# Kernel optimization log

Hardware: AMD Instinct MI355X
Metric: run time of the kernel (lower is better)

## Reference

```python
import jax, jax.numpy as jnp
import numpy as np

DIAG_MASK = 1e20  # value added on the diagonal to exclude self as negative


def setup_inputs() -> dict:
    key = jax.random.key(0)
    k1, k2, k3 = jax.random.split(key, 3)
    B, D_in, D_out = 4096, 1024, 1024
    anchor_x = jax.random.normal(k1, (B, D_in), dtype=jnp.float32)
    pos_x = jax.random.normal(k2, (B, D_in), dtype=jnp.float32)
    W = jax.random.normal(k3, (D_in, D_out), dtype=jnp.float32) * (1.0 / np.sqrt(D_in))
    b = jnp.zeros((D_out,), dtype=jnp.float32)
    return {"anchor_x": anchor_x, "pos_x": pos_x, "W": W, "b": b}


def reference(anchor_x, pos_x, W, b):
    # Encoder: simple dense projection (stand-in for the wrapped BERT encoder).
    anchor = anchor_x @ W + b          # [B, D]
    pos = pos_x @ W + b                # [B, D]

    # Pairwise squared distances dist[i,j] = ||anchor_i - pos_j||^2,
    # computed via the GEMM identity |a|^2 + |p|^2 - 2 a.p (same math as the
    # original broadcasted (a_i - p_j)^2 reduce_sum, far less memory traffic).
    a2 = jnp.sum(anchor * anchor, axis=-1, keepdims=True)       # [B, 1]
    p2 = jnp.sum(pos * pos, axis=-1, keepdims=True).T           # [1, B]
    dist = a2 + p2 - 2.0 * (anchor @ pos.T)                     # [B, B]

    B = dist.shape[0]
    mask_dist = dist + jnp.eye(B, dtype=dist.dtype) * DIAG_MASK  # mask diagonal
    indices = jnp.argmin(mask_dist, axis=-1)                     # [B] hard negatives
    neg = pos[indices]                                           # gather [B, D]

    return jnp.concatenate([anchor, pos, neg], axis=-1)          # [B, 3D]
```

## Files before the change

kernel.cpp:

```cpp
#include <hip/hip_runtime.h>


typedef short s8v __attribute__((ext_vector_type(8)));
typedef _Float16 h8v __attribute__((ext_vector_type(8)));
typedef float f4v __attribute__((ext_vector_type(4)));
typedef unsigned short u16;

#define B  4096
#define D  1024
#define OLD 3072
#define OLD16 6144
#define LDK 68

__device__ __forceinline__ u16 f2bf(float f) {
  union { float f; unsigned u; } v; v.f = f;
  unsigned r = v.u + 0x7FFFu + ((v.u >> 16) & 1u);
  return (u16)(r >> 16);
}
__device__ __forceinline__ float bf2f(u16 s) {
  union { unsigned u; float f; } v; v.u = ((unsigned)s) << 16;
  return v.f;
}

__device__ __forceinline__ void gld16(const void* g, void* l) {
  __builtin_amdgcn_global_load_lds(
      (const __attribute__((address_space(1))) unsigned int*)g,
      (__attribute__((address_space(3))) unsigned int*)l, 16, 0, 0);
}

struct Top2 { float v1, v2; int j1, j2; };
__device__ __forceinline__ void t2_insert(Top2& t, float v, int j) {
  if (v < t.v1 || (v == t.v1 && j < t.j1)) {
    t.v2 = t.v1; t.j2 = t.j1; t.v1 = v; t.j1 = j;
  } else if (v < t.v2 || (v == t.v2 && j < t.j2)) {
    t.v2 = v; t.j2 = j;
  }
}
struct Top4 { float v[4]; int j[4]; };
__device__ __forceinline__ void t4_insert(Top4& t, float v, int j) {
  if (v < t.v[3] || (v == t.v[3] && j < t.j[3])) {
    int p = 3;
#pragma unroll
    for (int s = 0; s < 3; ++s) {
      if (p > 0 && (v < t.v[p - 1] || (v == t.v[p - 1] && j < t.j[p - 1]))) {
        t.v[p] = t.v[p - 1]; t.j[p] = t.j[p - 1]; --p;
      }
    }
    t.v[p] = v; t.j[p] = j;
  }
}

__global__ void splitT_W(const float* __restrict__ W, u16* __restrict__ WtQ) {
  __shared__ float tile[32][33];
  const int bx = blockIdx.x * 32, by = blockIdx.y * 32;
  const int tx = threadIdx.x, ty = threadIdx.y;
  for (int dy = 0; dy < 32; dy += 8)
    tile[ty + dy][tx] = W[(size_t)(by + ty + dy) * D + bx + tx];
  __syncthreads();
  for (int dy = 0; dy < 32; dy += 8) {
    const float v = tile[tx][ty + dy];
    const u16 h = f2bf(v);
    const size_t o = (size_t)(bx + ty + dy) * 2048 + by + tx;
    WtQ[o] = h;
    WtQ[o + 1024] = f2bf(v - bf2f(h));
  }
}

__global__ __launch_bounds__(256) void splitX2(
    const float* __restrict__ A, const float* __restrict__ P,
    u16* __restrict__ O16, u16* __restrict__ posXq) {
  const int r = blockIdx.x, t = threadIdx.x;
  const bool isPos = r >= B;
  const int row = isPos ? r - B : r;
  const float4 v = *(const float4*)&(isPos ? P : A)[(size_t)row * D + t * 4];
  const float vv[4] = {v.x, v.y, v.z, v.w};
  ushort4 hi, mi;
  u16* hp = &hi.x; u16* mp = &mi.x;
#pragma unroll
  for (int i = 0; i < 4; ++i) {
    hp[i] = f2bf(vv[i]);
    mp[i] = f2bf(vv[i] - bf2f(hp[i]));
  }
  if (isPos) {
    *(ushort4*)&posXq[(size_t)row * 2048 + t * 4] = hi;
    *(ushort4*)&posXq[(size_t)row * 2048 + 1024 + t * 4] = mi;
  } else {
    *(ushort4*)&O16[(size_t)row * OLD16 + 4096 + t * 4] = hi;
    *(ushort4*)&O16[(size_t)row * OLD16 + 5120 + t * 4] = mi;
  }
}

__global__ __launch_bounds__(256) void enc_mfma(
    float* out, const u16* __restrict__ posXq, const u16* __restrict__ WtQ,
    const float* __restrict__ bias, _Float16* __restrict__ Aq,
    _Float16* __restrict__ Pq) {
  __shared__ __align__(16) u16 lAh[2][128 * 32], lAm[2][128 * 32];
  __shared__ __align__(16) u16 lBh[2][128 * 32], lBm[2][128 * 32];
  const u16* O16 = (const u16*)out;
  const int tid = threadIdx.x, lane = tid & 63, wave = tid >> 6;
  const int waveM = wave >> 1, waveN = wave & 1;
  const int row16 = lane & 15, quad = lane >> 4;
  const bool isPos = blockIdx.y >= 32;
  const int Mbase = (blockIdx.y & 31) * 128;
  const int Nbase = blockIdx.x * 128;
  f4v acc[4][4] = {};

  auto STAGE = [&](int buf, int kk) {
#pragma unroll
    for (int i = 0; i < 2; ++i) {
      const int c = i * 256 + tid;
      const int row = c >> 2;
      const int col8 = ((c & 3) ^ ((row >> 1) & 3)) * 8;
      u16* ah = &lAh[buf][(i * 256 + wave * 64) * 8];
      u16* am = &lAm[buf][(i * 256 + wave * 64) * 8];
      u16* bh = &lBh[buf][(i * 256 + wave * 64) * 8];
      u16* bm = &lBm[buf][(i * 256 + wave * 64) * 8];
      if (isPos) {
        gld16(&posXq[(size_t)(Mbase + row) * 2048 + kk + col8], ah);
        gld16(&posXq[(size_t)(Mbase + row) * 2048 + 1024 + kk + col8], am);
      } else {
        gld16(&O16[(size_t)(Mbase + row) * OLD16 + 4096 + kk + col8], ah);
        gld16(&O16[(size_t)(Mbase + row) * OLD16 + 5120 + kk + col8], am);
      }
      gld16(&WtQ[(size_t)(Nbase + row) * 2048 + kk + col8], bh);
      gld16(&WtQ[(size_t)(Nbase + row) * 2048 + 1024 + kk + col8], bm);
    }
  };

  STAGE(0, 0);
  __syncthreads();
  int cur = 0;
  const int slot = (quad ^ ((row16 >> 1) & 3)) * 8;
  for (int t = 1; t <= 32; ++t) {
    if (t < 32) STAGE(cur ^ 1, t * 32);
    s8v ah[4], am[4], bh[4], bm[4];
#pragma unroll
    for (int mi = 0; mi < 4; ++mi) {
      const int ro = (waveM * 64 + mi * 16 + row16) * 32 + slot;
      ah[mi] = *(const s8v*)&lAh[cur][ro];
      am[mi] = *(const s8v*)&lAm[cur][ro];
    }
#pragma unroll
    for (int ni = 0; ni < 4; ++ni) {
      const int ro = (waveN * 64 + ni * 16 + row16) * 32 + slot;
      bh[ni] = *(const s8v*)&lBh[cur][ro];
      bm[ni] = *(const s8v*)&lBm[cur][ro];
    }
#pragma unroll
    for (int mi = 0; mi < 4; ++mi)
#pragma unroll
      for (int ni = 0; ni < 4; ++ni) {
        f4v a = acc[mi][ni];
        a = __builtin_amdgcn_mfma_f32_16x16x32_bf16(ah[mi], bh[ni], a, 0, 0, 0);
        a = __builtin_amdgcn_mfma_f32_16x16x32_bf16(ah[mi], bm[ni], a, 0, 0, 0);
        a = __builtin_amdgcn_mfma_f32_16x16x32_bf16(am[mi], bh[ni], a, 0, 0, 0);
        acc[mi][ni] = a;
      }
    __syncthreads();
    cur ^= 1;
  }
  const int outOff = isPos ? 1024 : 0;
  _Float16* Q = isPos ? Pq : Aq;
#pragma unroll
  for (int ni = 0; ni < 4; ++ni) {
    const int col = Nbase + waveN * 64 + ni * 16 + row16;
    const float bv = bias[col];
#pragma unroll
    for (int mi = 0; mi < 4; ++mi) {
      const int rbase = Mbase + waveM * 64 + mi * 16 + quad * 4;
#pragma unroll
      for (int r = 0; r < 4; ++r) {
        const size_t row = rbase + r;
        const float v = acc[mi][ni][r] + bv;
        out[row * OLD + outOff + col] = v;
        Q[row * 1024 + col] = (_Float16)v;
      }
    }
  }
}

__global__ __launch_bounds__(256) void pnorm(float* __restrict__ o) {
  const int row = blockIdx.x, t = threadIdx.x;
  const float4 v = *(const float4*)&o[(size_t)row * OLD + D + t * 4];
  float s = v.x * v.x + v.y * v.y + v.z * v.z + v.w * v.w;
#pragma unroll
  for (int off = 32; off; off >>= 1) s += __shfl_down(s, off, 64);
  __shared__ float wsum[4];
  if ((t & 63) == 0) wsum[t >> 6] = s;
  __syncthreads();
  if (t == 0) o[(size_t)row * OLD + 2048] = wsum[0] + wsum[1] + wsum[2] + wsum[3];
}

__global__ __launch_bounds__(256) void dist_mfma(
    const _Float16* __restrict__ Aq, const _Float16* __restrict__ Pq,
    float* __restrict__ o) {
  __shared__ __align__(16) u16 lA[2][128 * 32];
  __shared__ __align__(16) u16 lB[2][128 * 32];
  __shared__ float sv1[128][2], sv2[128][2];
  __shared__ int sj1[128][2], sj2[128][2];
  const int tid = threadIdx.x, lane = tid & 63, wave = tid >> 6;
  const int waveM = wave >> 1, waveN = wave & 1;
  const int row16 = lane & 15, quad = lane >> 4;
  const int Mbase = blockIdx.y * 128;
  const int Nbase = blockIdx.x * 128;
  f4v acc[4][4] = {};

  auto STAGE = [&](int buf, int kk) {
#pragma unroll
    for (int i = 0; i < 2; ++i) {
      const int c = i * 256 + tid;
      const int row = c >> 2;
      const int col8 = ((c & 3) ^ ((row >> 1) & 3)) * 8;
      u16* la = &lA[buf][(i * 256 + wave * 64) * 8];
      u16* lb = &lB[buf][(i * 256 + wave * 64) * 8];
      gld16(&Aq[(size_t)(Mbase + row) * 1024 + kk + col8], la);
      gld16(&Pq[(size_t)(Nbase + row) * 1024 + kk + col8], lb);
    }
  };

  STAGE(0, 0);
  __syncthreads();
  int cur = 0;
  const int slot = (quad ^ ((row16 >> 1) & 3)) * 8;
  for (int t = 1; t <= 32; ++t) {
    if (t < 32) STAGE(cur ^ 1, t * 32);
    h8v a[4], b[4];
#pragma unroll
    for (int i = 0; i < 4; ++i) {
      a[i] = *(const h8v*)&lA[cur][(waveM * 64 + i * 16 + row16) * 32 + slot];
      b[i] = *(const h8v*)&lB[cur][(waveN * 64 + i * 16 + row16) * 32 + slot];
    }
#pragma unroll
    for (int mi = 0; mi < 4; ++mi)
#pragma unroll
      for (int ni = 0; ni < 4; ++ni)
        acc[mi][ni] =
            __builtin_amdgcn_mfma_f32_16x16x32_f16(a[mi], b[ni], acc[mi][ni], 0, 0, 0);
    __syncthreads();
    cur ^= 1;
  }

  float p2c[4];
#pragma unroll
  for (int ni = 0; ni < 4; ++ni)
    p2c[ni] = o[(size_t)(Nbase + waveN * 64 + ni * 16 + row16) * OLD + 2048];
#pragma unroll
  for (int mi = 0; mi < 4; ++mi)
#pragma unroll
    for (int r = 0; r < 4; ++r) {
      const int rg = Mbase + waveM * 64 + mi * 16 + quad * 4 + r;
      Top2 tp; tp.v1 = 3.0e38f; tp.v2 = 3.0e38f; tp.j1 = 0; tp.j2 = 1;
#pragma unroll
      for (int ni = 0; ni < 4; ++ni) {
        const int cg = Nbase + waveN * 64 + ni * 16 + row16;
        if (cg != rg) t2_insert(tp, p2c[ni] - 2.0f * acc[mi][ni][r], cg);
      }
#pragma unroll
      for (int m = 1; m < 16; m <<= 1) {
        const float ov1 = __shfl_xor(tp.v1, m, 64);
        const int oj1 = __shfl_xor(tp.j1, m, 64);
        const float ov2 = __shfl_xor(tp.v2, m, 64);
        const int oj2 = __shfl_xor(tp.j2, m, 64);
        t2_insert(tp, ov1, oj1);
        t2_insert(tp, ov2, oj2);
      }
      if (row16 == 0) {
        const int rl = waveM * 64 + mi * 16 + quad * 4 + r;
        sv1[rl][waveN] = tp.v1; sj1[rl][waveN] = tp.j1;
        sv2[rl][waveN] = tp.v2; sj2[rl][waveN] = tp.j2;
      }
    }
  __syncthreads();
  if (tid < 128) {
    Top2 tp; tp.v1 = sv1[tid][0]; tp.j1 = sj1[tid][0];
    tp.v2 = sv2[tid][0]; tp.j2 = sj2[tid][0];
    t2_insert(tp, sv1[tid][1], sj1[tid][1]);
    t2_insert(tp, sv2[tid][1], sj2[tid][1]);
    ((float4*)&o[(size_t)(Mbase + tid) * OLD + 2056])[blockIdx.x] =
        make_float4(tp.v1, __int_as_float(tp.j1), tp.v2, __int_as_float(tp.j2));
  }
}

__global__ __launch_bounds__(256) void argmin_refine(float* __restrict__ o) {
  const int i = blockIdx.x, t = threadIdx.x;
  __shared__ int gj[4];
  if (t < 64) {
    Top4 tp;
#pragma unroll
    for (int c = 0; c < 4; ++c) { tp.v[c] = 3.0e38f; tp.j[c] = 0; }
    if (t < 32) {
      const float4 p = ((const float4*)&o[(size_t)i * OLD + 2056])[t];
      t4_insert(tp, p.x, __float_as_int(p.y));
      t4_insert(tp, p.z, __float_as_int(p.w));
    }
#pragma unroll
    for (int m = 1; m < 32; m <<= 1) {
#pragma unroll
      for (int c = 0; c < 4; ++c) {
        const float ov = __shfl_xor(tp.v[c], m, 64);
        const int oj = __shfl_xor(tp.j[c], m, 64);
        t4_insert(tp, ov, oj);
      }
    }
    if (t == 0) {
#pragma unroll
      for (int c = 0; c < 4; ++c)
        gj[c] = (tp.j[c] < 0) ? 0 : (tp.j[c] > B - 1 ? B - 1 : tp.j[c]);
    }
  }
  __syncthreads();
  int jj[4];
#pragma unroll
  for (int c = 0; c < 4; ++c) jj[c] = gj[c];
  const float4 a4 = *(const float4*)&o[(size_t)i * OLD + t * 4];
  float s[4], n[4];
#pragma unroll
  for (int c = 0; c < 4; ++c) {
    const float4 q = *(const float4*)&o[(size_t)jj[c] * OLD + D + t * 4];
    s[c] = a4.x * q.x + a4.y * q.y + a4.z * q.z + a4.w * q.w;
    n[c] = q.x * q.x + q.y * q.y + q.z * q.z + q.w * q.w;
  }
#pragma unroll
  for (int off = 32; off; off >>= 1)
#pragma unroll
    for (int c = 0; c < 4; ++c) {
      s[c] += __shfl_down(s[c], off, 64);
      n[c] += __shfl_down(n[c], off, 64);
    }
  __shared__ float wsum[4][8];
  __shared__ int sjf;
  if ((t & 63) == 0)
#pragma unroll
    for (int c = 0; c < 4; ++c) {
      wsum[t >> 6][c] = s[c];
      wsum[t >> 6][4 + c] = n[c];
    }
  __syncthreads();
  if (t == 0) {
    float bd = 3.4e38f; int bj = 0x7fffffff;
#pragma unroll
    for (int c = 0; c < 4; ++c) {
      const float S = wsum[0][c] + wsum[1][c] + wsum[2][c] + wsum[3][c];
      const float N = wsum[0][4 + c] + wsum[1][4 + c] + wsum[2][4 + c] + wsum[3][4 + c];
      const float d = N - 2.0f * S;
      const int j = jj[c];
      if (d < bd || (d == bd && j < bj)) { bd = d; bj = j; }
    }
    sjf = bj;
  }
  __syncthreads();
  const int j = sjf;
  ((float4*)&o[(size_t)i * OLD + 2048])[t] = ((const float4*)&o[(size_t)j * OLD + D])[t];
}

__global__ __launch_bounds__(256) void enc_gemm(
    const float* __restrict__ X, const float* __restrict__ W,
    const float* __restrict__ bia, float* __restrict__ out, int outOff) {
  __shared__ float lA[32][LDK];
  __shared__ float lW[32][LDK];
  const int tid = threadIdx.x;
  const int Mbase = blockIdx.y * 64;
  const int Nbase = blockIdx.x * 64;
  const int ty = tid >> 4, tx = tid & 15;
  float acc[4][4] = {};
  for (int k0 = 0; k0 < D; k0 += 32) {
    __syncthreads();
#pragma unroll
    for (int h = 0; h < 2; ++h) {
      const int ch = tid + h * 256;
      const int r = ch >> 3, c4 = (ch & 7) * 4;
      const float4 a4 = *(const float4*)&X[(size_t)(Mbase + r) * D + k0 + c4];
      lA[c4 + 0][r] = a4.x; lA[c4 + 1][r] = a4.y;
      lA[c4 + 2][r] = a4.z; lA[c4 + 3][r] = a4.w;
      const int kr = ch >> 4, nc = (ch & 15) * 4;
      *(float4*)&lW[kr][nc] = *(const float4*)&W[(size_t)(k0 + kr) * D + Nbase + nc];
    }
    __syncthreads();
#pragma unroll
    for (int kk = 0; kk < 32; ++kk) {
      const float4 av = *(const float4*)&lA[kk][ty * 4];
      const float4 wv = *(const float4*)&lW[kk][tx * 4];
      acc[0][0] += av.x * wv.x; acc[0][1] += av.x * wv.y; acc[0][2] += av.x * wv.z; acc[0][3] += av.x * wv.w;
      acc[1][0] += av.y * wv.x; acc[1][1] += av.y * wv.y; acc[1][2] += av.y * wv.z; acc[1][3] += av.y * wv.w;
      acc[2][0] += av.z * wv.x; acc[2][1] += av.z * wv.y; acc[2][2] += av.z * wv.z; acc[2][3] += av.z * wv.w;
      acc[3][0] += av.w * wv.x; acc[3][1] += av.w * wv.y; acc[3][2] += av.w * wv.z; acc[3][3] += av.w * wv.w;
    }
  }
  const float4 b4 = *(const float4*)&bia[Nbase + tx * 4];
#pragma unroll
  for (int i = 0; i < 4; ++i) {
    const int row = Mbase + ty * 4 + i;
    float4 ov;
    ov.x = acc[i][0] + b4.x; ov.y = acc[i][1] + b4.y;
    ov.z = acc[i][2] + b4.z; ov.w = acc[i][3] + b4.w;
    *(float4*)&out[(size_t)row * OLD + outOff + Nbase + tx * 4] = ov;
  }
}

__global__ __launch_bounds__(256) void dist_argmin_f32(float* __restrict__ o) {
  __shared__ float lA[32][LDK];
  __shared__ float lB[32][LDK];
  const int tid = threadIdx.x;
  const int Mbase = blockIdx.y * 64, Nbase = blockIdx.x * 64;
  const int ty = tid >> 4, tx = tid & 15;
  float acc[4][4] = {};
  for (int k0 = 0; k0 < D; k0 += 32) {
    __syncthreads();
#pragma unroll
    for (int h = 0; h < 2; ++h) {
      const int ch = tid + h * 256;
      const int r = ch >> 3, c4 = (ch & 7) * 4;
      const float4 a4 = *(const float4*)&o[(size_t)(Mbase + r) * OLD + k0 + c4];
      const float4 b4 = *(const float4*)&o[(size_t)(Nbase + r) * OLD + D + k0 + c4];
      lA[c4 + 0][r] = a4.x; lA[c4 + 1][r] = a4.y;
      lA[c4 + 2][r] = a4.z; lA[c4 + 3][r] = a4.w;
      lB[c4 + 0][r] = b4.x; lB[c4 + 1][r] = b4.y;
      lB[c4 + 2][r] = b4.z; lB[c4 + 3][r] = b4.w;
    }
    __syncthreads();
#pragma unroll
    for (int kk = 0; kk < 32; ++kk) {
      const float4 av = *(const float4*)&lA[kk][ty * 4];
      const float4 bv = *(const float4*)&lB[kk][tx * 4];
      acc[0][0] += av.x * bv.x; acc[0][1] += av.x * bv.y; acc[0][2] += av.x * bv.z; acc[0][3] += av.x * bv.w;
      acc[1][0] += av.y * bv.x; acc[1][1] += av.y * bv.y; acc[1][2] += av.y * bv.z; acc[1][3] += av.y * bv.w;
      acc[2][0] += av.z * bv.x; acc[2][1] += av.z * bv.y; acc[2][2] += av.z * bv.z; acc[2][3] += av.z * bv.w;
      acc[3][0] += av.w * bv.x; acc[3][1] += av.w * bv.y; acc[3][2] += av.w * bv.z; acc[3][3] += av.w * bv.w;
    }
  }
  float colp2[4];
#pragma unroll
  for (int j = 0; j < 4; ++j)
    colp2[j] = o[(size_t)(Nbase + tx * 4 + j) * OLD + 2048];
#pragma unroll
  for (int i = 0; i < 4; ++i) {
    const int rg = Mbase + ty * 4 + i;
    float bv = 3.0e38f; int bj = 0;
#pragma unroll
    for (int j = 0; j < 4; ++j) {
      const int cg = Nbase + tx * 4 + j;
      const float d = colp2[j] - 2.0f * acc[i][j];
      if (cg != rg && d < bv) { bv = d; bj = cg; }
    }
#pragma unroll
    for (int m = 1; m < 16; m <<= 1) {
      const float ov = __shfl_xor(bv, m, 64);
      const int oj = __shfl_xor(bj, m, 64);
      if (ov < bv || (ov == bv && oj < bj)) { bv = ov; bj = oj; }
    }
    if (tx == 0)
      ((float2*)&o[(size_t)rg * OLD + 2056])[blockIdx.x] =
          make_float2(bv, __int_as_float(bj));
  }
}

__global__ __launch_bounds__(256) void argmin_final_f2(float* __restrict__ o, int nblk) {
  const int i = blockIdx.x, t = threadIdx.x;
  __shared__ int sj;
  if (t < 64) {
    float v = 3.4e38f; int j = 0x7fffffff;
    if (t < nblk) {
      const float2 p = ((const float2*)&o[(size_t)i * OLD + 2056])[t];
      v = p.x; j = __float_as_int(p.y);
    }
#pragma unroll
    for (int m = 32; m; m >>= 1) {
      const float ov = __shfl_xor(v, m, 64);
      const int oj = __shfl_xor(j, m, 64);
      if (ov < v || (ov == v && oj < j)) { v = ov; j = oj; }
    }
    if (t == 0) sj = (j < 0) ? 0 : (j > B - 1 ? B - 1 : j);
  }
  __syncthreads();
  const int j = sj;
  ((float4*)&o[(size_t)i * OLD + 2048])[t] = ((const float4*)&o[(size_t)j * OLD + D])[t];
}

extern "C" void kernel_launch(void* const* d_in, const int* in_sizes, int n_in,
                              void* d_out, int out_size, void* d_ws, size_t ws_size,
                              hipStream_t stream) {
  const float* anchor_x = (const float*)d_in[0];
  const float* pos_x    = (const float*)d_in[1];
  const float* W        = (const float*)d_in[2];
  const float* b        = (const float*)d_in[3];
  float* out = (float*)d_out;
  char* ws = (char*)d_ws;
  const size_t MB = 1024 * 1024;

  if (ws_size >= 36 * MB) {
    _Float16* Aq = (_Float16*)(ws);
    _Float16* Pq = (_Float16*)(ws + 8 * MB);
    u16* WtQ     = (u16*)(ws + 16 * MB);
    u16* posXq   = (u16*)(ws + 20 * MB);
    splitT_W<<<dim3(32, 32), dim3(32, 8), 0, stream>>>(W, WtQ);
    splitX2<<<2 * B, 256, 0, stream>>>(anchor_x, pos_x, (u16*)out, posXq);
    enc_mfma<<<dim3(8, 64), 256, 0, stream>>>(out, posXq, WtQ, b, Aq, Pq);
    pnorm<<<B, 256, 0, stream>>>(out);
    dist_mfma<<<dim3(32, 32), 256, 0, stream>>>(Aq, Pq, out);
    argmin_refine<<<B, 256, 0, stream>>>(out);
  } else {
    enc_gemm<<<dim3(16, 64), 256, 0, stream>>>(anchor_x, W, b, out, 0);
    enc_gemm<<<dim3(16, 64), 256, 0, stream>>>(pos_x,    W, b, out, 1024);
    pnorm<<<B, 256, 0, stream>>>(out);
    dist_argmin_f32<<<dim3(64, 64), 256, 0, stream>>>(out);
    argmin_final_f2<<<B, 256, 0, stream>>>(out, 64);
  }
}
```

Measured before the change: 343.4 us.

## Enlarge dist GEMM tile to 256x256 and single-buffer encoder GEMM

The distance GEMM moves from 128x128 tiles with 4 waves to 256x256 tiles with 8 waves, each wave holding an 8x4 MFMA accumulator block. The cross-wave top-2 merge now covers 4 N-waves, and argmin_refine reads 16 partial candidates instead of 32. The larger tile is meant to raise operand reuse and cut global and LDS traffic per FLOP, at the cost of more registers, more LDS and fewer blocks. Separately, the encoder GEMM drops double buffering for a single LDS buffer with two barriers per k-step. This halves its LDS use but serializes loads and MFMA work.

```diff
diff --git a/kernel.cpp b/kernel.cpp
--- a/kernel.cpp
+++ b/kernel.cpp
@@ -94,8 +94,8 @@
     float* out, const u16* __restrict__ posXq, const u16* __restrict__ WtQ,
     const float* __restrict__ bias, _Float16* __restrict__ Aq,
     _Float16* __restrict__ Pq) {
-  __shared__ __align__(16) u16 lAh[2][128 * 32], lAm[2][128 * 32];
-  __shared__ __align__(16) u16 lBh[2][128 * 32], lBm[2][128 * 32];
+  __shared__ __align__(16) u16 lAh[128 * 32], lAm[128 * 32];
+  __shared__ __align__(16) u16 lBh[128 * 32], lBm[128 * 32];
   const u16* O16 = (const u16*)out;
   const int tid = threadIdx.x, lane = tid & 63, wave = tid >> 6;
   const int waveM = wave >> 1, waveN = wave & 1;
@@ -104,47 +104,39 @@
   const int Mbase = (blockIdx.y & 31) * 128;
   const int Nbase = blockIdx.x * 128;
   f4v acc[4][4] = {};
-
-  auto STAGE = [&](int buf, int kk) {
+  const int slot = (quad ^ ((row16 >> 1) & 3)) * 8;
+
+  for (int kk = 0; kk < D; kk += 32) {
+    __syncthreads();
 #pragma unroll
     for (int i = 0; i < 2; ++i) {
       const int c = i * 256 + tid;
       const int row = c >> 2;
       const int col8 = ((c & 3) ^ ((row >> 1) & 3)) * 8;
-      u16* ah = &lAh[buf][(i * 256 + wave * 64) * 8];
-      u16* am = &lAm[buf][(i * 256 + wave * 64) * 8];
-      u16* bh = &lBh[buf][(i * 256 + wave * 64) * 8];
-      u16* bm = &lBm[buf][(i * 256 + wave * 64) * 8];
+      const int lo = (i * 256 + wave * 64) * 8;
       if (isPos) {
-        gld16(&posXq[(size_t)(Mbase + row) * 2048 + kk + col8], ah);
-        gld16(&posXq[(size_t)(Mbase + row) * 2048 + 1024 + kk + col8], am);
+        gld16(&posXq[(size_t)(Mbase + row) * 2048 + kk + col8], &lAh[lo]);
+        gld16(&posXq[(size_t)(Mbase + row) * 2048 + 1024 + kk + col8], &lAm[lo]);
       } else {
-        gld16(&O16[(size_t)(Mbase + row) * OLD16 + 4096 + kk + col8], ah);
-        gld16(&O16[(size_t)(Mbase + row) * OLD16 + 5120 + kk + col8], am);
-      }
-      gld16(&WtQ[(size_t)(Nbase + row) * 2048 + kk + col8], bh);
-      gld16(&WtQ[(size_t)(Nbase + row) * 2048 + 1024 + kk + col8], bm);
-    }
-  };
-
-  STAGE(0, 0);
-  __syncthreads();
-  int cur = 0;
-  const int slot = (quad ^ ((row16 >> 1) & 3)) * 8;
-  for (int t = 1; t <= 32; ++t) {
-    if (t < 32) STAGE(cur ^ 1, t * 32);
+        gld16(&O16[(size_t)(Mbase + row) * OLD16 + 4096 + kk + col8], &lAh[lo]);
+        gld16(&O16[(size_t)(Mbase + row) * OLD16 + 5120 + kk + col8], &lAm[lo]);
+      }
+      gld16(&WtQ[(size_t)(Nbase + row) * 2048 + kk + col8], &lBh[lo]);
+      gld16(&WtQ[(size_t)(Nbase + row) * 2048 + 1024 + kk + col8], &lBm[lo]);
+    }
+    __syncthreads();
     s8v ah[4], am[4], bh[4], bm[4];
 #pragma unroll
     for (int mi = 0; mi < 4; ++mi) {
       const int ro = (waveM * 64 + mi * 16 + row16) * 32 + slot;
-      ah[mi] = *(const s8v*)&lAh[cur][ro];
-      am[mi] = *(const s8v*)&lAm[cur][ro];
+      ah[mi] = *(const s8v*)&lAh[ro];
+      am[mi] = *(const s8v*)&lAm[ro];
     }
 #pragma unroll
     for (int ni = 0; ni < 4; ++ni) {
       const int ro = (waveN * 64 + ni * 16 + row16) * 32 + slot;
-      bh[ni] = *(const s8v*)&lBh[cur][ro];
-      bm[ni] = *(const s8v*)&lBm[cur][ro];
+      bh[ni] = *(const s8v*)&lBh[ro];
+      bm[ni] = *(const s8v*)&lBm[ro];
     }
 #pragma unroll
     for (int mi = 0; mi < 4; ++mi)
@@ -156,8 +148,6 @@
         a = __builtin_amdgcn_mfma_f32_16x16x32_bf16(am[mi], bh[ni], a, 0, 0, 0);
         acc[mi][ni] = a;
       }
-    __syncthreads();
-    cur ^= 1;
   }
   const int outOff = isPos ? 1024 : 0;
   _Float16* Q = isPos ? Pq : Aq;
@@ -191,28 +181,28 @@
   if (t == 0) o[(size_t)row * OLD + 2048] = wsum[0] + wsum[1] + wsum[2] + wsum[3];
 }
 
-__global__ __launch_bounds__(256) void dist_mfma(
+__global__ __launch_bounds__(512, 2) void dist_mfma(
     const _Float16* __restrict__ Aq, const _Float16* __restrict__ Pq,
     float* __restrict__ o) {
-  __shared__ __align__(16) u16 lA[2][128 * 32];
-  __shared__ __align__(16) u16 lB[2][128 * 32];
-  __shared__ float sv1[128][2], sv2[128][2];
-  __shared__ int sj1[128][2], sj2[128][2];
+  __shared__ __align__(16) u16 lA[2][256 * 32];
+  __shared__ __align__(16) u16 lB[2][256 * 32];
+  __shared__ float sv1[256][4], sv2[256][4];
+  __shared__ int sj1[256][4], sj2[256][4];
   const int tid = threadIdx.x, lane = tid & 63, wave = tid >> 6;
-  const int waveM = wave >> 1, waveN = wave & 1;
+  const int waveM = wave >> 2, waveN = wave & 3;
   const int row16 = lane & 15, quad = lane >> 4;
-  const int Mbase = blockIdx.y * 128;
-  const int Nbase = blockIdx.x * 128;
-  f4v acc[4][4] = {};
+  const int Mbase = blockIdx.y * 256;
+  const int Nbase = blockIdx.x * 256;
+  f4v acc[8][4] = {};
 
   auto STAGE = [&](int buf, int kk) {
 #pragma unroll
     for (int i = 0; i < 2; ++i) {
-      const int c = i * 256 + tid;
+      const int c = i * 512 + tid;
       const int row = c >> 2;
       const int col8 = ((c & 3) ^ ((row >> 1) & 3)) * 8;
-      u16* la = &lA[buf][(i * 256 + wave * 64) * 8];
-      u16* lb = &lB[buf][(i * 256 + wave * 64) * 8];
+      u16* la = &lA[buf][(i * 512 + wave * 64) * 8];
+      u16* lb = &lB[buf][(i * 512 + wave * 64) * 8];
       gld16(&Aq[(size_t)(Mbase + row) * 1024 + kk + col8], la);
       gld16(&Pq[(size_t)(Nbase + row) * 1024 + kk + col8], lb);
     }
@@ -224,14 +214,15 @@
   const int slot = (quad ^ ((row16 >> 1) & 3)) * 8;
   for (int t = 1; t <= 32; ++t) {
     if (t < 32) STAGE(cur ^ 1, t * 32);
-    h8v a[4], b[4];
-#pragma unroll
-    for (int i = 0; i < 4; ++i) {
-      a[i] = *(const h8v*)&lA[cur][(waveM * 64 + i * 16 + row16) * 32 + slot];
-      b[i] = *(const h8v*)&lB[cur][(waveN * 64 + i * 16 + row16) * 32 + slot];
-    }
-#pragma unroll
-    for (int mi = 0; mi < 4; ++mi)
+    h8v a[8], b[4];
+#pragma unroll
+    for (int mi = 0; mi < 8; ++mi)
+      a[mi] = *(const h8v*)&lA[cur][(waveM * 128 + mi * 16 + row16) * 32 + slot];
+#pragma unroll
+    for (int ni = 0; ni < 4; ++ni)
+      b[ni] = *(const h8v*)&lB[cur][(waveN * 64 + ni * 16 + row16) * 32 + slot];
+#pragma unroll
+    for (int mi = 0; mi < 8; ++mi)
 #pragma unroll
       for (int ni = 0; ni < 4; ++ni)
         acc[mi][ni] =
@@ -245,10 +236,10 @@
   for (int ni = 0; ni < 4; ++ni)
     p2c[ni] = o[(size_t)(Nbase + waveN * 64 + ni * 16 + row16) * OLD + 2048];
 #pragma unroll
-  for (int mi = 0; mi < 4; ++mi)
+  for (int mi = 0; mi < 8; ++mi)
 #pragma unroll
     for (int r = 0; r < 4; ++r) {
-      const int rg = Mbase + waveM * 64 + mi * 16 + quad * 4 + r;
+      const int rg = Mbase + waveM * 128 + mi * 16 + quad * 4 + r;
       Top2 tp; tp.v1 = 3.0e38f; tp.v2 = 3.0e38f; tp.j1 = 0; tp.j2 = 1;
 #pragma unroll
       for (int ni = 0; ni < 4; ++ni) {
@@ -265,17 +256,20 @@
         t2_insert(tp, ov2, oj2);
       }
       if (row16 == 0) {
-        const int rl = waveM * 64 + mi * 16 + quad * 4 + r;
+        const int rl = waveM * 128 + mi * 16 + quad * 4 + r;
         sv1[rl][waveN] = tp.v1; sj1[rl][waveN] = tp.j1;
         sv2[rl][waveN] = tp.v2; sj2[rl][waveN] = tp.j2;
       }
     }
   __syncthreads();
-  if (tid < 128) {
+  if (tid < 256) {
     Top2 tp; tp.v1 = sv1[tid][0]; tp.j1 = sj1[tid][0];
     tp.v2 = sv2[tid][0]; tp.j2 = sj2[tid][0];
-    t2_insert(tp, sv1[tid][1], sj1[tid][1]);
-    t2_insert(tp, sv2[tid][1], sj2[tid][1]);
+#pragma unroll
+    for (int w = 1; w < 4; ++w) {
+      t2_insert(tp, sv1[tid][w], sj1[tid][w]);
+      t2_insert(tp, sv2[tid][w], sj2[tid][w]);
+    }
     ((float4*)&o[(size_t)(Mbase + tid) * OLD + 2056])[blockIdx.x] =
         make_float4(tp.v1, __int_as_float(tp.j1), tp.v2, __int_as_float(tp.j2));
   }
@@ -288,7 +282,7 @@
     Top4 tp;
 #pragma unroll
     for (int c = 0; c < 4; ++c) { tp.v[c] = 3.0e38f; tp.j[c] = 0; }
-    if (t < 32) {
+    if (t < 16) {
       const float4 p = ((const float4*)&o[(size_t)i * OLD + 2056])[t];
       t4_insert(tp, p.x, __float_as_int(p.y));
       t4_insert(tp, p.z, __float_as_int(p.w));
@@ -496,7 +490,7 @@
     splitX2<<<2 * B, 256, 0, stream>>>(anchor_x, pos_x, (u16*)out, posXq);
     enc_mfma<<<dim3(8, 64), 256, 0, stream>>>(out, posXq, WtQ, b, Aq, Pq);
     pnorm<<<B, 256, 0, stream>>>(out);
-    dist_mfma<<<dim3(32, 32), 256, 0, stream>>>(Aq, Pq, out);
+    dist_mfma<<<dim3(16, 16), 512, 0, stream>>>(Aq, Pq, out);
     argmin_refine<<<B, 256, 0, stream>>>(out);
   } else {
     enc_gemm<<<dim3(16, 64), 256, 0, stream>>>(anchor_x, W, b, out, 0);
```

Result: faster. 287.1 us, median of 2 (-16.4%).
